# Kernel tuning notes

Hardware: AMD Instinct MI355X
Metric: run time of the kernel (lower is better)

Reference implementation:

```python
import jax, jax.numpy as jnp
import numpy as np

EPS = 1e-12

def setup_inputs() -> dict:
    key = jax.random.key(0)
    k1, k2, k3 = jax.random.split(key, 3)
    B, D, N, NCLS = 1024, 512, 100000, 1000
    z = jax.random.normal(k1, (B, D), dtype=jnp.float32)
    lab_bank = jax.random.normal(k2, (N, D), dtype=jnp.float32)
    lab_labels = jax.random.randint(k3, (N,), 0, NCLS, dtype=jnp.int64)
    return {"z": z, "lab_bank": lab_bank, "lab_labels": lab_labels, "topk": 5}

def reference(z, lab_bank, lab_labels, topk):
    # cosine similarity: normalize query and bank, then GEMM
    zn = z / jnp.maximum(jnp.linalg.norm(z, axis=-1, keepdims=True), EPS)            # [B, D]
    bn = lab_bank / jnp.maximum(jnp.linalg.norm(lab_bank, axis=-1, keepdims=True), EPS)  # [N, D]
    sim = jnp.einsum('bd,nd->bn', zn, bn)                                            # [B, N]
    top_vals, top_idx = jax.lax.top_k(sim, topk)                                     # [B, k] each
    labels = lab_labels[top_idx]                                                     # [B, k]
    return top_idx, top_vals, labels
```

## Files before the change

### kernel.cpp

```cpp
#include <hip/hip_runtime.h>
#include <math.h>

#define DDIM 512
#define NS 96
#define KMASK 0xFFFFF800
#define NEG_INF (-3.0e38f)
#define IMAX 0x7fffffff

typedef _Float16 f16x8 __attribute__((ext_vector_type(8)));
typedef float    f32x4 __attribute__((ext_vector_type(4)));
typedef int      i32x4 __attribute__((ext_vector_type(4)));

__device__ __forceinline__ int imin(int a, int b) { return a < b ? a : b; }
__device__ __forceinline__ int imax(int a, int b) { return a > b ? a : b; }

__device__ __forceinline__ int med3(int a, int b, int c) {
    int d;
    asm("v_med3_i32 %0, %1, %2, %3" : "=v"(d) : "v"(a), "v"(b), "v"(c));
    return d;
}

__device__ __forceinline__ void glds16(const void* g, void* l) {
    __builtin_amdgcn_global_load_lds((const __attribute__((address_space(1))) void*)g,
                                     (__attribute__((address_space(3))) void*)l, 16, 0, 0);
}

#define KBAR() do { asm volatile("s_waitcnt vmcnt(0)" ::: "memory"); \
                    __builtin_amdgcn_s_barrier();                    \
                    asm volatile("" ::: "memory"); } while (0)

__global__ __launch_bounds__(256) void split_tile_k(
    const float* __restrict__ zsrc, const float* __restrict__ bsrc,
    unsigned* __restrict__ ztile, unsigned* __restrict__ btile,
    float* __restrict__ rz, float* __restrict__ rb,
    int zrows, int brows, int nbBlocks) {

    const int bx = blockIdx.x;
    const float* src; unsigned* tile; float* rn; int rows; int blk;
    if (bx < nbBlocks) { src = bsrc; tile = btile; rn = rb; rows = brows; blk = bx; }
    else               { src = zsrc; tile = ztile; rn = rz; rows = zrows; blk = bx - nbBlocks; }

    const int t = threadIdx.x;
    const int r = t >> 1, hf = t & 1;
    const int R = blk * 128 + r;
    const bool valid = R < rows;
    const float* srow = src + (size_t)(valid ? R : 0) * DDIM + hf * 16;

    float ss = 0.f;
    for (int ks = 0; ks < 16; ++ks) {
        float4 v0 = *(const float4*)(srow + ks * 32);
        float4 v1 = *(const float4*)(srow + ks * 32 + 4);
        float4 v2 = *(const float4*)(srow + ks * 32 + 8);
        float4 v3 = *(const float4*)(srow + ks * 32 + 12);
        ss += v0.x*v0.x + v0.y*v0.y + v0.z*v0.z + v0.w*v0.w
            + v1.x*v1.x + v1.y*v1.y + v1.z*v1.z + v1.w*v1.w
            + v2.x*v2.x + v2.y*v2.y + v2.z*v2.z + v2.w*v2.w
            + v3.x*v3.x + v3.y*v3.y + v3.z*v3.z + v3.w*v3.w;
        unsigned o[8];
        o[0] = __builtin_bit_cast(unsigned, __builtin_amdgcn_cvt_pkrtz(v0.x, v0.y));
        o[1] = __builtin_bit_cast(unsigned, __builtin_amdgcn_cvt_pkrtz(v0.z, v0.w));
        o[2] = __builtin_bit_cast(unsigned, __builtin_amdgcn_cvt_pkrtz(v1.x, v1.y));
        o[3] = __builtin_bit_cast(unsigned, __builtin_amdgcn_cvt_pkrtz(v1.z, v1.w));
        o[4] = __builtin_bit_cast(unsigned, __builtin_amdgcn_cvt_pkrtz(v2.x, v2.y));
        o[5] = __builtin_bit_cast(unsigned, __builtin_amdgcn_cvt_pkrtz(v2.z, v2.w));
        o[6] = __builtin_bit_cast(unsigned, __builtin_amdgcn_cvt_pkrtz(v3.x, v3.y));
        o[7] = __builtin_bit_cast(unsigned, __builtin_amdgcn_cvt_pkrtz(v3.z, v3.w));
        if (!valid) {
            #pragma unroll
            for (int q = 0; q < 8; ++q) o[q] = 0u;
        }
        unsigned* dst = tile + (size_t)(blk * 16 + ks) * 2048
                             + (r >> 4) * 256 + (hf * 32 + (r & 15)) * 4;
        *(i32x4*)dst        = *(i32x4*)o;
        *(i32x4*)(dst + 64) = *(i32x4*)(o + 4);
    }
    ss += __shfl_xor(ss, 1, 64);
    if (hf == 0) rn[R] = valid ? 1.0f / fmaxf(sqrtf(ss), 1e-12f) : 0.0f;
}

__global__ __launch_bounds__(256, 4) void gemm_screen_k(
    const unsigned* __restrict__ zh, const unsigned* __restrict__ bh,
    const float* __restrict__ rb,
    int* __restrict__ cand, int N, int nChunks) {

    __shared__ alignas(16) int smem[8192];

    const int t = threadIdx.x;
    const int w = t >> 6, lane = t & 63;
    const int wz = w >> 1, wb = w & 1;
    const int quad = lane >> 4, l16 = lane & 15;
    const int split = blockIdx.x, rowblk = blockIdx.y;
    const int soff = w * 1024 + lane * 16;

    int T[4][4];
    #pragma unroll
    for (int zi = 0; zi < 4; ++zi)
        #pragma unroll
        for (int q = 0; q < 4; ++q) T[zi][q] = (int)0x80000000;

    {
        const char* gA = (const char*)zh + (size_t)(rowblk * 16) * 8192;
        const char* gB = (const char*)bh + (size_t)(split * 16) * 8192;
        glds16(gA + soff,        (char*)smem + soff);
        glds16(gA + 4096 + soff, (char*)smem + 4096 + soff);
        glds16(gB + soff,        (char*)smem + 8192 + soff);
        glds16(gB + 4096 + soff, (char*)smem + 12288 + soff);
    }

    int iter = 0;
    for (int chunk = split; chunk < nChunks; chunk += NS, ++iter) {
        f32x4 acc[4][4];
        #pragma unroll
        for (int bi = 0; bi < 4; ++bi)
            #pragma unroll
            for (int zi = 0; zi < 4; ++zi) acc[bi][zi] = (f32x4){0.f, 0.f, 0.f, 0.f};
        f32x4 rbv[4];

        #pragma unroll 2
        for (int ks = 0; ks < 16; ++ks) {
            KBAR();
            if (ks < 15) {
                const char* gA = (const char*)zh + (size_t)(rowblk * 16 + ks + 1) * 8192;
                const char* gB = (const char*)bh + (size_t)(chunk * 16 + ks + 1) * 8192;
                char* l = (char*)smem + (((ks & 1) ^ 1) << 14);
                glds16(gA + soff,        l + soff);
                glds16(gA + 4096 + soff, l + 4096 + soff);
                glds16(gB + soff,        l + 8192 + soff);
                glds16(gB + 4096 + soff, l + 12288 + soff);
            } else if (chunk + NS < nChunks) {
                const char* gA = (const char*)zh + (size_t)(rowblk * 16) * 8192;
                const char* gB = (const char*)bh + (size_t)((chunk + NS) * 16) * 8192;
                glds16(gA + soff,        (char*)smem + soff);
                glds16(gA + 4096 + soff, (char*)smem + 4096 + soff);
                glds16(gB + soff,        (char*)smem + 8192 + soff);
                glds16(gB + 4096 + soff, (char*)smem + 12288 + soff);
            }
            if (ks == 0) {
                #pragma unroll
                for (int bi = 0; bi < 4; ++bi)
                    rbv[bi] = *(const f32x4*)(rb + chunk * 128 + wb * 64 + bi * 16 + quad * 4);
            }

            const char* Ab = (const char*)smem + ((ks & 1) << 14);
            const char* Bb = Ab + 8192;
            f16x8 af[4], bf[4];
            #pragma unroll
            for (int zi = 0; zi < 4; ++zi)
                af[zi] = __builtin_bit_cast(f16x8,
                    *(const i32x4*)(Ab + (wz * 4 + zi) * 1024 + quad * 256 + l16 * 16));
            #pragma unroll
            for (int bi = 0; bi < 4; ++bi)
                bf[bi] = __builtin_bit_cast(f16x8,
                    *(const i32x4*)(Bb + (wb * 4 + bi) * 1024 + quad * 256 + l16 * 16));
            #pragma unroll
            for (int bi = 0; bi < 4; ++bi)
                #pragma unroll
                for (int zi = 0; zi < 4; ++zi)
                    acc[bi][zi] = __builtin_amdgcn_mfma_f32_16x16x32_f16(bf[bi], af[zi], acc[bi][zi], 0, 0, 0);
        }

        const int tbase = (iter << 7) | (wb << 6) | (quad << 2);
        #pragma unroll
        for (int zi = 0; zi < 4; ++zi)
            #pragma unroll
            for (int bi = 0; bi < 4; ++bi)
                #pragma unroll
                for (int rr = 0; rr < 4; ++rr) {
                    float v = acc[bi][zi][rr] * rbv[bi][rr];
                    int kk = (__float_as_int(v) & KMASK) | (tbase + bi * 16 + rr);
                    int n1 = med3(kk, T[zi][0], T[zi][1]);
                    int n2 = med3(kk, T[zi][1], T[zi][2]);
                    int n3 = med3(kk, T[zi][2], T[zi][3]);
                    T[zi][0] = imax(kk, T[zi][0]);
                    T[zi][1] = n1; T[zi][2] = n2; T[zi][3] = n3;
                }
    }

    #pragma unroll
    for (int zi = 0; zi < 4; ++zi) {
        int a0 = T[zi][0], a1 = T[zi][1], a2 = T[zi][2], a3 = T[zi][3];
        #pragma unroll
        for (int off = 16; off <= 32; off <<= 1) {
            int p0 = __shfl_xor(a0, off, 64);
            int p1 = __shfl_xor(a1, off, 64);
            int p2 = __shfl_xor(a2, off, 64);
            int p3 = __shfl_xor(a3, off, 64);
            int m0 = imax(a0, p3), m1 = imax(a1, p2), m2 = imax(a2, p1), m3 = imax(a3, p0);
            int b0 = imax(m0, m2), b2 = imin(m0, m2), b1 = imax(m1, m3), b3 = imin(m1, m3);
            a0 = imax(b0, b1); a1 = imin(b0, b1); a2 = imax(b2, b3); a3 = imin(b2, b3);
        }
        if (quad == 0) {
            i32x4 outk = { a0, a1, a2, a3 };
            const int row = rowblk * 128 + wz * 64 + zi * 16 + l16;
            *(i32x4*)(cand + (((size_t)row * NS + split) * 2 + wb) * 4) = outk;
        }
    }
}

__global__ __launch_bounds__(256) void merge_rescore_k(
    const int* __restrict__ cand,
    const float* __restrict__ z, const float* __restrict__ bank,
    const float* __restrict__ rz, const float* __restrict__ rb,
    const int* __restrict__ labels, float* __restrict__ out, int BK, int N) {

    __shared__ float zrow[DDIM];
    __shared__ int   idxs[32];
    __shared__ float dots[32];

    const int row = blockIdx.x;
    const int t = threadIdx.x, w = t >> 6, lane = t & 63;

    {   float2 v = *(const float2*)(z + (size_t)row * DDIM + t * 2);
        zrow[t * 2] = v.x; zrow[t * 2 + 1] = v.y; }

    if (w == 0) {
        int k[12];
        const int* cp = cand + (size_t)row * (NS * 2 * 4) + lane * 12;
        #pragma unroll
        for (int q = 0; q < 12; ++q) k[q] = cp[q];
        for (int r = 0; r < 32; ++r) {
            int lk = k[0], lq = 0;
            #pragma unroll
            for (int q = 1; q < 12; ++q) if (k[q] > lk) { lk = k[q]; lq = q; }
            int wk = lk, wl = lane, wq = lq;
            #pragma unroll
            for (int off = 32; off > 0; off >>= 1) {
                int ok = __shfl_xor(wk, off, 64);
                int ol = __shfl_xor(wl, off, 64);
                int oq = __shfl_xor(wq, off, 64);
                if (ok > wk || (ok == wk && ol < wl)) { wk = ok; wl = ol; wq = oq; }
            }
            if (lane == wl) {
                #pragma unroll
                for (int q = 0; q < 12; ++q) if (q == wq) k[q] = (int)0x80000000;
            }
            if (lane == 0) {
                int j = wl * 12 + wq;
                int split = j >> 3;
                int c = wk & 127, it = (wk >> 7) & 15;
                int gi = (it * NS + split) * 128 + c;
                idxs[r] = gi < N ? gi : 0;
            }
        }
    }
    __syncthreads();

    #pragma unroll
    for (int jj = 0; jj < 8; ++jj) {
        const int ci = idxs[w * 8 + jj];
        const float* br = bank + (size_t)ci * DDIM + lane * 8;
        float4 x0 = *(const float4*)br;
        float4 x1 = *(const float4*)(br + 4);
        const float* zz = zrow + lane * 8;
        float4 z0 = *(const float4*)zz;
        float4 z1 = *(const float4*)(zz + 4);
        float s = x0.x*z0.x + x0.y*z0.y + x0.z*z0.z + x0.w*z0.w
                + x1.x*z1.x + x1.y*z1.y + x1.z*z1.z + x1.w*z1.w;
        #pragma unroll
        for (int off = 32; off > 0; off >>= 1) s += __shfl_xor(s, off, 64);
        if (lane == 0) dots[w * 8 + jj] = s;
    }
    __syncthreads();

    if (w == 0) {
        const float rzv = rz[row];
        float v; int ii;
        if (lane < 32) { ii = idxs[lane]; v = dots[lane] * rzv * rb[ii]; }
        else           { ii = IMAX;       v = NEG_INF; }
        for (int r = 0; r < 5; ++r) {
            float bv = v; int bi = ii;
            #pragma unroll
            for (int off = 32; off > 0; off >>= 1) {
                float ov = __shfl_xor(bv, off, 64);
                int   oi = __shfl_xor(bi, off, 64);
                if (ov > bv || (ov == bv && oi < bi)) { bv = ov; bi = oi; }
            }
            if (v == bv && ii == bi) { v = NEG_INF; ii = IMAX; }
            if (lane == 0) {
                out[(size_t)row * 5 + r]          = (float)bi;
                out[BK + (size_t)row * 5 + r]     = bv;
                out[2 * BK + (size_t)row * 5 + r] = (float)labels[bi];
            }
        }
    }
}

extern "C" void kernel_launch(void* const* d_in, const int* in_sizes, int n_in,
                              void* d_out, int out_size, void* d_ws, size_t ws_size,
                              hipStream_t stream) {
    const float* z    = (const float*)d_in[0];
    const float* bank = (const float*)d_in[1];
    const int*   lab  = (const int*)d_in[2];
    const int B = in_sizes[0] / DDIM;
    const int N = in_sizes[1] / DDIM;
    const int BK = out_size / 3;
    const int nChunks = (N + 127) >> 7;
    float* out = (float*)d_out;
    char* ws = (char*)d_ws;

    const size_t o_rz = 0;
    const size_t o_rb = 4096;
    const size_t o_zh = o_rb + (size_t)nChunks * 128 * 4;
    const size_t o_bh = o_zh + (size_t)(B / 128) * 16 * 8192;
    const size_t o_cv = o_bh + (size_t)nChunks * 16 * 8192;

    float* rz = (float*)(ws + o_rz);
    float* rb = (float*)(ws + o_rb);
    unsigned* zh = (unsigned*)(ws + o_zh);
    unsigned* bh = (unsigned*)(ws + o_bh);
    int* cand = (int*)(ws + o_cv);

    split_tile_k<<<nChunks + B / 128, 256, 0, stream>>>(z, bank, zh, bh, rz, rb, B, N, nChunks);
    gemm_screen_k<<<dim3(NS, B / 128), 256, 0, stream>>>(zh, bh, rb, cand, N, nChunks);
    merge_rescore_k<<<B, 256, 0, stream>>>(cand, z, bank, rz, rb, lab, out, BK, N);
}
```

Baseline: 469.6 us.

## Triple-buffer LDS staging in GEMM screen with partial vmcnt waits

Replaces the double-buffered LDS pipeline with a three-buffer ring that prefetches two k-steps ahead, across chunk boundaries. Each barrier now waits with vmcnt(4) or vmcnt(8) instead of vmcnt(0), so the next stage's global-to-LDS loads can stay in flight while the current tile is computed. The last stages issue dummy reloads to keep the outstanding-load count fixed. The k-loop is fully unrolled, and LDS grows to 48KB per block with launch bounds lowered from 4 to 3 blocks per CU, which trades occupancy for deeper latency hiding.

```diff
diff --git a/kernel.cpp b/kernel.cpp
--- a/kernel.cpp
+++ b/kernel.cpp
@@ -25,9 +25,12 @@
                                      (__attribute__((address_space(3))) void*)l, 16, 0, 0);
 }
 
-#define KBAR() do { asm volatile("s_waitcnt vmcnt(0)" ::: "memory"); \
-                    __builtin_amdgcn_s_barrier();                    \
-                    asm volatile("" ::: "memory"); } while (0)
+#define KBAR4() do { asm volatile("s_waitcnt vmcnt(4)" ::: "memory"); \
+                     __builtin_amdgcn_s_barrier();                    \
+                     asm volatile("" ::: "memory"); } while (0)
+#define KBAR8() do { asm volatile("s_waitcnt vmcnt(8)" ::: "memory"); \
+                     __builtin_amdgcn_s_barrier();                    \
+                     asm volatile("" ::: "memory"); } while (0)
 
 __global__ __launch_bounds__(256) void split_tile_k(
     const float* __restrict__ zsrc, const float* __restrict__ bsrc,
@@ -78,12 +81,12 @@
     if (hf == 0) rn[R] = valid ? 1.0f / fmaxf(sqrtf(ss), 1e-12f) : 0.0f;
 }
 
-__global__ __launch_bounds__(256, 4) void gemm_screen_k(
+__global__ __launch_bounds__(256, 3) void gemm_screen_k(
     const unsigned* __restrict__ zh, const unsigned* __restrict__ bh,
     const float* __restrict__ rb,
     int* __restrict__ cand, int N, int nChunks) {
 
-    __shared__ alignas(16) int smem[8192];
+    __shared__ alignas(16) int smem[12288];
 
     const int t = threadIdx.x;
     const int w = t >> 6, lane = t & 63;
@@ -98,14 +101,21 @@
         #pragma unroll
         for (int q = 0; q < 4; ++q) T[zi][q] = (int)0x80000000;
 
-    {
-        const char* gA = (const char*)zh + (size_t)(rowblk * 16) * 8192;
-        const char* gB = (const char*)bh + (size_t)(split * 16) * 8192;
-        glds16(gA + soff,        (char*)smem + soff);
-        glds16(gA + 4096 + soff, (char*)smem + 4096 + soff);
-        glds16(gB + soff,        (char*)smem + 8192 + soff);
-        glds16(gB + 4096 + soff, (char*)smem + 12288 + soff);
-    }
+    char* pr = (char*)smem;
+    char* pn = (char*)smem + 16384;
+    char* pw = (char*)smem + 32768;
+
+    #define STAGE(KK, CC, DST) do {                                              \
+        const char* gA_ = (const char*)zh + (size_t)(rowblk * 16 + (KK)) * 8192; \
+        const char* gB_ = (const char*)bh + (size_t)((CC) * 16 + (KK)) * 8192;   \
+        glds16(gA_ + soff,        (DST) + soff);                                 \
+        glds16(gA_ + 4096 + soff, (DST) + 4096 + soff);                          \
+        glds16(gB_ + soff,        (DST) + 8192 + soff);                          \
+        glds16(gB_ + 4096 + soff, (DST) + 12288 + soff);                         \
+    } while (0)
+
+    STAGE(0, split, pr);
+    STAGE(1, split, pn);
 
     int iter = 0;
     for (int chunk = split; chunk < nChunks; chunk += NS, ++iter) {
@@ -116,47 +126,38 @@
             for (int zi = 0; zi < 4; ++zi) acc[bi][zi] = (f32x4){0.f, 0.f, 0.f, 0.f};
         f32x4 rbv[4];
 
-        #pragma unroll 2
+        #pragma unroll
         for (int ks = 0; ks < 16; ++ks) {
-            KBAR();
-            if (ks < 15) {
-                const char* gA = (const char*)zh + (size_t)(rowblk * 16 + ks + 1) * 8192;
-                const char* gB = (const char*)bh + (size_t)(chunk * 16 + ks + 1) * 8192;
-                char* l = (char*)smem + (((ks & 1) ^ 1) << 14);
-                glds16(gA + soff,        l + soff);
-                glds16(gA + 4096 + soff, l + 4096 + soff);
-                glds16(gB + soff,        l + 8192 + soff);
-                glds16(gB + 4096 + soff, l + 12288 + soff);
-            } else if (chunk + NS < nChunks) {
-                const char* gA = (const char*)zh + (size_t)(rowblk * 16) * 8192;
-                const char* gB = (const char*)bh + (size_t)((chunk + NS) * 16) * 8192;
-                glds16(gA + soff,        (char*)smem + soff);
-                glds16(gA + 4096 + soff, (char*)smem + 4096 + soff);
-                glds16(gB + soff,        (char*)smem + 8192 + soff);
-                glds16(gB + 4096 + soff, (char*)smem + 12288 + soff);
-            }
+            if (ks == 1) KBAR8(); else KBAR4();
+
             if (ks == 0) {
                 #pragma unroll
                 for (int bi = 0; bi < 4; ++bi)
                     rbv[bi] = *(const f32x4*)(rb + chunk * 128 + wb * 64 + bi * 16 + quad * 4);
             }
-
-            const char* Ab = (const char*)smem + ((ks & 1) << 14);
-            const char* Bb = Ab + 8192;
+            {
+                int tk = ks + 2, tc = chunk;
+                if (tk > 15) { tk -= 16; tc += NS; }
+                if (tc >= nChunks) { tk = ks; tc = chunk; }
+                STAGE(tk, tc, pw);
+            }
+
             f16x8 af[4], bf[4];
             #pragma unroll
             for (int zi = 0; zi < 4; ++zi)
                 af[zi] = __builtin_bit_cast(f16x8,
-                    *(const i32x4*)(Ab + (wz * 4 + zi) * 1024 + quad * 256 + l16 * 16));
+                    *(const i32x4*)(pr + (wz * 4 + zi) * 1024 + quad * 256 + l16 * 16));
             #pragma unroll
             for (int bi = 0; bi < 4; ++bi)
                 bf[bi] = __builtin_bit_cast(f16x8,
-                    *(const i32x4*)(Bb + (wb * 4 + bi) * 1024 + quad * 256 + l16 * 16));
+                    *(const i32x4*)(pr + 8192 + (wb * 4 + bi) * 1024 + quad * 256 + l16 * 16));
             #pragma unroll
             for (int bi = 0; bi < 4; ++bi)
                 #pragma unroll
                 for (int zi = 0; zi < 4; ++zi)
                     acc[bi][zi] = __builtin_amdgcn_mfma_f32_16x16x32_f16(bf[bi], af[zi], acc[bi][zi], 0, 0, 0);
+
+            char* tp = pr; pr = pn; pn = pw; pw = tp;
         }
 
         const int tbase = (iter << 7) | (wb << 6) | (quad << 2);
@@ -175,6 +176,7 @@
                     T[zi][1] = n1; T[zi][2] = n2; T[zi][3] = n3;
                 }
     }
+    #undef STAGE
 
     #pragma unroll
     for (int zi = 0; zi < 4; ++zi) {
```

Measured after the change: 492.2 us. +4.8%, slower.

## Load query tile directly from global into registers, stage only bank tile in LDS

Applied to the files above, without the earlier changes.

The query (A) fragments are now read straight from global memory into registers each k-step instead of being staged through LDS. Only the bank (B) slab is double-buffered in shared memory, which halves the LDS footprint. Launch bounds drop from 4 to 3 blocks per SM, allowing more registers per thread. This removes LDS traffic and staging for A, but the A loads now sit on the critical path with no prefetch, so each k-step is exposed to global/L2 latency.

```diff
diff --git a/kernel.cpp b/kernel.cpp
--- a/kernel.cpp
+++ b/kernel.cpp
@@ -78,19 +78,19 @@
     if (hf == 0) rn[R] = valid ? 1.0f / fmaxf(sqrtf(ss), 1e-12f) : 0.0f;
 }
 
-__global__ __launch_bounds__(256, 4) void gemm_screen_k(
+__global__ __launch_bounds__(256, 3) void gemm_screen_k(
     const unsigned* __restrict__ zh, const unsigned* __restrict__ bh,
     const float* __restrict__ rb,
     int* __restrict__ cand, int N, int nChunks) {
 
-    __shared__ alignas(16) int smem[8192];
+    __shared__ alignas(16) int smem[4096];
 
     const int t = threadIdx.x;
     const int w = t >> 6, lane = t & 63;
     const int wz = w >> 1, wb = w & 1;
     const int quad = lane >> 4, l16 = lane & 15;
     const int split = blockIdx.x, rowblk = blockIdx.y;
-    const int soff = w * 1024 + lane * 16;
+    const int soff = t * 16;
 
     int T[4][4];
     #pragma unroll
@@ -98,14 +98,13 @@
         #pragma unroll
         for (int q = 0; q < 4; ++q) T[zi][q] = (int)0x80000000;
 
-    {
-        const char* gA = (const char*)zh + (size_t)(rowblk * 16) * 8192;
-        const char* gB = (const char*)bh + (size_t)(split * 16) * 8192;
-        glds16(gA + soff,        (char*)smem + soff);
-        glds16(gA + 4096 + soff, (char*)smem + 4096 + soff);
-        glds16(gB + soff,        (char*)smem + 8192 + soff);
-        glds16(gB + 4096 + soff, (char*)smem + 12288 + soff);
-    }
+    #define STAGE_B(SLAB, DST) do {                                        \
+        const char* gB_ = (const char*)bh + (size_t)(SLAB) * 8192;         \
+        glds16(gB_ + soff,        (DST) + soff);                           \
+        glds16(gB_ + 4096 + soff, (DST) + 4096 + soff);                    \
+    } while (0)
+
+    STAGE_B((size_t)split * 16, (char*)smem);
 
     int iter = 0;
     for (int chunk = split; chunk < nChunks; chunk += NS, ++iter) {
@@ -119,21 +118,18 @@
         #pragma unroll 2
         for (int ks = 0; ks < 16; ++ks) {
             KBAR();
+
+            const char* gA = (const char*)zh + (size_t)(rowblk * 16 + ks) * 8192;
+            f16x8 af[4];
+            #pragma unroll
+            for (int zi = 0; zi < 4; ++zi)
+                af[zi] = __builtin_bit_cast(f16x8,
+                    *(const i32x4*)(gA + (wz * 4 + zi) * 1024 + quad * 256 + l16 * 16));
+
             if (ks < 15) {
-                const char* gA = (const char*)zh + (size_t)(rowblk * 16 + ks + 1) * 8192;
-                const char* gB = (const char*)bh + (size_t)(chunk * 16 + ks + 1) * 8192;
-                char* l = (char*)smem + (((ks & 1) ^ 1) << 14);
-                glds16(gA + soff,        l + soff);
-                glds16(gA + 4096 + soff, l + 4096 + soff);
-                glds16(gB + soff,        l + 8192 + soff);
-                glds16(gB + 4096 + soff, l + 12288 + soff);
+                STAGE_B((size_t)chunk * 16 + ks + 1, (char*)smem + (((ks & 1) ^ 1) << 13));
             } else if (chunk + NS < nChunks) {
-                const char* gA = (const char*)zh + (size_t)(rowblk * 16) * 8192;
-                const char* gB = (const char*)bh + (size_t)((chunk + NS) * 16) * 8192;
-                glds16(gA + soff,        (char*)smem + soff);
-                glds16(gA + 4096 + soff, (char*)smem + 4096 + soff);
-                glds16(gB + soff,        (char*)smem + 8192 + soff);
-                glds16(gB + 4096 + soff, (char*)smem + 12288 + soff);
+                STAGE_B((size_t)(chunk + NS) * 16, (char*)smem);
             }
             if (ks == 0) {
                 #pragma unroll
@@ -141,13 +137,8 @@
                     rbv[bi] = *(const f32x4*)(rb + chunk * 128 + wb * 64 + bi * 16 + quad * 4);
             }
 
-            const char* Ab = (const char*)smem + ((ks & 1) << 14);
-            const char* Bb = Ab + 8192;
-            f16x8 af[4], bf[4];
-            #pragma unroll
-            for (int zi = 0; zi < 4; ++zi)
-                af[zi] = __builtin_bit_cast(f16x8,
-                    *(const i32x4*)(Ab + (wz * 4 + zi) * 1024 + quad * 256 + l16 * 16));
+            const char* Bb = (const char*)smem + ((ks & 1) << 13);
+            f16x8 bf[4];
             #pragma unroll
             for (int bi = 0; bi < 4; ++bi)
                 bf[bi] = __builtin_bit_cast(f16x8,
@@ -175,6 +166,7 @@
                     T[zi][1] = n1; T[zi][2] = n2; T[zi][3] = n3;
                 }
     }
+    #undef STAGE_B
 
     #pragma unroll
     for (int zi = 0; zi < 4; ++zi) {
```

After: 466.2 us. Within noise of the previous version (-0.7%).
